# Performance work log

Hardware: AMD Instinct MI355X
Metric: run time of the kernel (lower is better)

The kernel has to match this reference:

```python
import jax, jax.numpy as jnp
import numpy as np

N_ATOMS = 300000
D_IN = 256


def setup_inputs() -> dict:
    key = jax.random.key(0)
    ks = jax.random.split(key, 8)

    def xavier(k, fan_in, fan_out):
        limit = float(np.sqrt(6.0 / (fan_in + fan_out)))
        return jax.random.uniform(k, (fan_in, fan_out), jnp.float32, -limit, limit)

    density = jax.random.normal(ks[0], (N_ATOMS, D_IN), jnp.float32)
    species = jax.random.randint(ks[1], (N_ATOMS,), -1, 10, jnp.int64)
    return {
        "density": density,
        "species": species,
        "W1": xavier(ks[2], 256, 512), "b1": jnp.zeros((512,), jnp.float32),
        "W2": xavier(ks[3], 512, 512), "b2": jnp.zeros((512,), jnp.float32),
        "W3": xavier(ks[4], 512, 256), "b3": jnp.zeros((256,), jnp.float32),
        "W4": xavier(ks[5], 256, 1),   "b4": jnp.zeros((1,), jnp.float32),
    }


def reference(density, species, W1, b1, W2, b2, W3, b3, W4, b4):
    # Equivalent to torch's nonzero-gather -> MLP -> scatter into zeros:
    # compute the MLP on all rows, then zero rows where species <= -0.5.
    h = jax.nn.silu(density @ W1 + b1)   # [N, 512]
    h = jax.nn.silu(h @ W2 + b2)         # [N, 512]
    h = jax.nn.silu(h @ W3 + b3)         # [N, 256]
    out = h @ W4 + b4                    # [N, 1]
    mask = species > -0.5                # valid atoms
    return jnp.where(mask[:, None], out, jnp.zeros((), out.dtype))
```

## Files before the change

kernel.cpp:

```cpp
#include <hip/hip_runtime.h>

typedef _Float16 half8 __attribute__((ext_vector_type(8)));
typedef _Float16 half4 __attribute__((ext_vector_type(4)));
typedef float f32x4 __attribute__((ext_vector_type(4)));
typedef float f32x16 __attribute__((ext_vector_type(16)));

#define NCHUNK_MAX 2048

__global__ void prep_compact(const float* __restrict__ W1, const float* __restrict__ W2,
                             const float* __restrict__ W3, const float* __restrict__ W4,
                             _Float16* __restrict__ wt1, _Float16* __restrict__ wt2,
                             _Float16* __restrict__ wt3, _Float16* __restrict__ w4h,
                             const int* __restrict__ species, int* __restrict__ idxloc,
                             int* __restrict__ cnt, float* __restrict__ out,
                             int natoms, int nprep) {
  __shared__ int wsum[4];
  if (blockIdx.x >= nprep) {
    const int c = blockIdx.x - nprep;
    const int i = c * 256 + threadIdx.x;
    const bool valid = (i < natoms) && (species[i] >= 0);
    const unsigned long long m = __ballot(valid);
    const int lane = threadIdx.x & 63, w = threadIdx.x >> 6;
    if (lane == 0) wsum[w] = (int)__popcll(m);
    __syncthreads();
    int base = 0;
#pragma unroll
    for (int k = 0; k < 4; ++k)
      if (k < w) base += wsum[k];
    if (valid) {
      int off = (int)__popcll(m & ((1ull << lane) - 1));
      idxloc[c * 256 + base + off] = i;
    } else if (i < natoms) {
      out[i] = 0.0f;
    }
    if (threadIdx.x == 0) cnt[c] = wsum[0] + wsum[1] + wsum[2] + wsum[3];
    return;
  }
  int idx = blockIdx.x * blockDim.x + threadIdx.x;
  if (idx < 512 * 256) {
    int k = idx >> 9, n = idx & 511;
    int off = (((n >> 5) * 16 + (k >> 4)) << 9) + (n & 31) * 8 + (((k >> 3) & 1) << 8) + (k & 7);
    wt1[off] = (_Float16)W1[idx];
    return;
  }
  int i2 = idx - 512 * 256;
  if (i2 < 512 * 512) {
    int k = i2 >> 9, n = i2 & 511;
    int off = (((n >> 5) * 32 + (k >> 4)) << 9) + (n & 31) * 8 + (((k >> 3) & 1) << 8) + (k & 7);
    wt2[off] = (_Float16)W2[i2];
    return;
  }
  int i3 = i2 - 512 * 512;
  if (i3 < 512 * 256) {
    int k = i3 >> 8, n = i3 & 255;
    int off = (((n >> 5) * 32 + (k >> 4)) << 9) + (n & 31) * 8 + (((k >> 3) & 1) << 8) + (k & 7);
    wt3[off] = (_Float16)W3[i3];
    return;
  }
  int i4 = i3 - 512 * 256;
  if (i4 < 256) w4h[i4] = (_Float16)W4[i4];
}

__device__ __forceinline__ float fast_silu(float s) {
  float e = __expf(-s);
  float d = 1.0f + e;
  float r;
  asm("v_rcp_f32 %0, %1" : "=v"(r) : "v"(d));
  return s * r;
}


#define MFMA(a, b, c) __builtin_amdgcn_mfma_f32_32x32x16_f16(a, b, c, 0, 0, 0)

template <int FT, int AT, int KS, int PIN, int POUT>
__device__ __forceinline__ void layer(const _Float16* __restrict__ wt,
                                      const float* __restrict__ bias,
                                      char* __restrict__ Hb,
                                      int wfeat, int lane) {
  const int lr = lane & 31;
  const int lh = lane >> 5;
  const int n0 = wfeat * (FT * 32);
  const int s0 = (lr & 31) << 4;
  const char* Bp = Hb + lr * PIN;
  const char* wp = (const char*)wt + (size_t)(wfeat * FT * KS) * 1024 + lh * 512 + lr * 16;

  f32x16 acc[FT][AT];
#pragma unroll
  for (int f = 0; f < FT; ++f)
#pragma unroll
    for (int rg = 0; rg < 4; ++rg) {
      const int feat = n0 + f * 32 + rg * 8 + lh * 4;
      const f32x4 bv = *(const f32x4*)(bias + feat);
#pragma unroll
      for (int a = 0; a < AT; ++a)
#pragma unroll
        for (int r = 0; r < 4; ++r) acc[f][a][rg * 4 + r] = bv[r];
    }

  half8 Af[FT], Ag[FT], Bf[AT], Bg[AT];
#pragma unroll
  for (int f = 0; f < FT; ++f) Af[f] = *(const half8*)(wp + f * (KS * 1024));
#pragma unroll
  for (int a = 0; a < AT; ++a)
    Bf[a] = *(const half8*)(Bp + a * 32 * PIN + ((lh * 16) ^ s0));

#pragma unroll 1
  for (int ks = 0; ks < KS - 2; ks += 2) {
#pragma unroll
    for (int f = 0; f < FT; ++f)
      Ag[f] = *(const half8*)(wp + f * (KS * 1024) + (ks + 1) * 1024);
#pragma unroll
    for (int a = 0; a < AT; ++a)
      Bg[a] = *(const half8*)(Bp + a * 32 * PIN + (((ks + 1) * 32 + lh * 16) ^ s0));
#pragma unroll
    for (int f = 0; f < FT; ++f)
#pragma unroll
      for (int a = 0; a < AT; ++a) acc[f][a] = MFMA(Af[f], Bf[a], acc[f][a]);
#pragma unroll
    for (int f = 0; f < FT; ++f)
      Af[f] = *(const half8*)(wp + f * (KS * 1024) + (ks + 2) * 1024);
#pragma unroll
    for (int a = 0; a < AT; ++a)
      Bf[a] = *(const half8*)(Bp + a * 32 * PIN + (((ks + 2) * 32 + lh * 16) ^ s0));
#pragma unroll
    for (int f = 0; f < FT; ++f)
#pragma unroll
      for (int a = 0; a < AT; ++a) acc[f][a] = MFMA(Ag[f], Bg[a], acc[f][a]);
  }
#pragma unroll
  for (int f = 0; f < FT; ++f)
    Ag[f] = *(const half8*)(wp + f * (KS * 1024) + (KS - 1) * 1024);
#pragma unroll
  for (int a = 0; a < AT; ++a)
    Bg[a] = *(const half8*)(Bp + a * 32 * PIN + ((((KS - 1) * 32) + lh * 16) ^ s0));
#pragma unroll
  for (int f = 0; f < FT; ++f)
#pragma unroll
    for (int a = 0; a < AT; ++a) acc[f][a] = MFMA(Af[f], Bf[a], acc[f][a]);
#pragma unroll
  for (int f = 0; f < FT; ++f)
#pragma unroll
    for (int a = 0; a < AT; ++a) acc[f][a] = MFMA(Ag[f], Bg[a], acc[f][a]);

#pragma unroll
  for (int f = 0; f < FT; ++f)
#pragma unroll
    for (int a = 0; a < AT; ++a)
#pragma unroll
      for (int j = 0; j < 16; ++j) acc[f][a][j] = fast_silu(acc[f][a][j]);

  __syncthreads();

#pragma unroll
  for (int f = 0; f < FT; ++f) {
#pragma unroll
    for (int rg = 0; rg < 4; ++rg) {
      const int feat = n0 + f * 32 + rg * 8 + lh * 4;
#pragma unroll
      for (int a = 0; a < AT; ++a) {
        half4 h;
#pragma unroll
        for (int r = 0; r < 4; ++r) h[r] = (_Float16)acc[f][a][rg * 4 + r];
        const int row = a * 32 + lr;
        *(half4*)(Hb + row * POUT + ((feat * 2) ^ ((row & 31) << 4))) = h;
      }
    }
  }
}

extern "C" __global__ void __launch_bounds__(512, 4)
mlp_kernel(const float* __restrict__ X, const int* __restrict__ species,
           const _Float16* __restrict__ wt1, const float* __restrict__ b1,
           const _Float16* __restrict__ wt2, const float* __restrict__ b2,
           const _Float16* __restrict__ wt3, const float* __restrict__ b3,
           const _Float16* __restrict__ w4h, const float* __restrict__ b4,
           float* __restrict__ out, int natoms,
           const int* __restrict__ idxloc, const int* __restrict__ cnt, int nchunks) {
  __shared__ __align__(16) char H[64 * 1024];
  __shared__ int prefixS[NCHUNK_MAX + 1];
  __shared__ int gidx[64];
  __shared__ int wtot[8];
  const int tid = threadIdx.x;
  const int lane = tid & 63;
  const int wid = tid >> 6;
  const long abase = (long)blockIdx.x * 64;

  int nvalid = natoms;
  if (idxloc) {
    int v[4];
    int tsum = 0;
#pragma unroll
    for (int j = 0; j < 4; ++j) {
      const int c = tid * 4 + j;
      v[j] = (c < nchunks) ? cnt[c] : 0;
      tsum += v[j];
    }
    int ws_ = tsum;
#pragma unroll
    for (int d = 1; d < 64; d <<= 1) {
      int o = __shfl_up(ws_, d);
      if (lane >= d) ws_ += o;
    }
    if (lane == 63) wtot[wid] = ws_;
    __syncthreads();
    int wbase = 0, tot = 0;
#pragma unroll
    for (int k = 0; k < 8; ++k) {
      if (k < wid) wbase += wtot[k];
      tot += wtot[k];
    }
    int run = wbase + ws_ - tsum;
#pragma unroll
    for (int j = 0; j < 4; ++j) {
      const int c = tid * 4 + j;
      if (c < nchunks) prefixS[c] = run;
      run += v[j];
    }
    if (tid == 0) prefixS[nchunks] = tot;
    nvalid = tot;
    __syncthreads();
    if (abase >= nvalid) return;
  }

  {
    const int r = tid >> 3, cg = tid & 7;
    long li = abase + r;
    const long lmax = (long)nvalid - 1;
    if (li > lmax) li = lmax;
    long g = li;
    if (idxloc) {
      int lo = 0, hi = nchunks - 1;
      while (lo < hi) {
        int mid = (lo + hi + 1) >> 1;
        if (prefixS[mid] <= (int)li) lo = mid; else hi = mid - 1;
      }
      g = idxloc[lo * 256 + ((int)li - prefixS[lo])];
      if (cg == 0) gidx[r] = (int)g;
    }
    const float* xp = X + g * 256;
    const int sw = (r & 31) << 4;
#pragma unroll
    for (int j = 0; j < 8; ++j) {
      const int colh = cg * 4 + j * 32;
      f32x4 v = *(const f32x4*)(xp + colh);
      half4 h;
#pragma unroll
      for (int e = 0; e < 4; ++e) h[e] = (_Float16)v[e];
      *(half4*)(H + r * 512 + ((colh * 2) ^ sw)) = h;
    }
  }
  __syncthreads();

  layer<2, 2, 16, 512, 1024>(wt1, b1, H, wid, lane);
  __syncthreads();
  layer<2, 2, 32, 1024, 1024>(wt2, b2, H, wid, lane);
  __syncthreads();
  layer<1, 2, 32, 1024, 1024>(wt3, b3, H, wid, lane);
  __syncthreads();

  const int atom = tid >> 3, part = tid & 7;
  const int sw = (atom & 31) << 4;
  const char* h3 = H + atom * 1024;
  const _Float16* w4p = w4h + part * 32;
  float sum = 0.0f;
#pragma unroll
  for (int j = 0; j < 4; ++j) {
    half8 h = *(const half8*)(h3 + ((part * 64 + j * 16) ^ sw));
    half8 w = *(const half8*)(w4p + j * 8);
#pragma unroll
    for (int e = 0; e < 8; ++e) sum += (float)h[e] * (float)w[e];
  }
  sum += __shfl_xor(sum, 1);
  sum += __shfl_xor(sum, 2);
  sum += __shfl_xor(sum, 4);
  if (part == 0) {
    const long li = abase + atom;
    if (li < nvalid) {
      float r = sum + b4[0];
      if (idxloc) {
        out[gidx[atom]] = r;
      } else {
        out[li] = (species[li] >= 0) ? r : 0.0f;
      }
    }
  }
}

extern "C" void kernel_launch(void* const* d_in, const int* in_sizes, int n_in,
                              void* d_out, int out_size, void* d_ws, size_t ws_size,
                              hipStream_t stream) {
  const float* X = (const float*)d_in[0];
  const int* species = (const int*)d_in[1];
  const float* W1 = (const float*)d_in[2];
  const float* b1 = (const float*)d_in[3];
  const float* W2 = (const float*)d_in[4];
  const float* b2 = (const float*)d_in[5];
  const float* W3 = (const float*)d_in[6];
  const float* b3 = (const float*)d_in[7];
  const float* W4 = (const float*)d_in[8];
  const float* b4 = (const float*)d_in[9];
  float* out = (float*)d_out;
  const int natoms = in_sizes[0] / 256;

  char* ws = (char*)d_ws;
  _Float16* wt1 = (_Float16*)(ws);
  _Float16* wt2 = (_Float16*)(ws + 262144);
  _Float16* wt3 = (_Float16*)(ws + 262144 + 524288);
  _Float16* w4h = (_Float16*)(ws + 262144 + 524288 + 262144);
  int* cnt = (int*)(ws + 1049088);
  int* idxloc = (int*)(ws + 1049088 + 8192);

  const int nchunks = (natoms + 255) / 256;
  const size_t ws_needed = 1049088 + 8192 + (size_t)natoms * 4;
  const bool use_compact = (ws_size >= ws_needed) && (nchunks <= NCHUNK_MAX);

  const int prep_total = 512 * 256 + 512 * 512 + 256 * 512 + 256;
  const int nprep = (prep_total + 255) / 256;
  const int nblk = nprep + (use_compact ? nchunks : 0);
  hipLaunchKernelGGL(prep_compact, dim3(nblk), dim3(256), 0, stream,
                     W1, W2, W3, W4, wt1, wt2, wt3, w4h,
                     species, idxloc, cnt, out, natoms, nprep);

  const int nblocks = (natoms + 63) / 64;
  hipLaunchKernelGGL(mlp_kernel, dim3(nblocks), dim3(512), 0, stream,
                     X, species, wt1, b1, wt2, b2, wt3, b3, w4h, b4, out, natoms,
                     use_compact ? idxloc : (const int*)nullptr,
                     use_compact ? (const int*)cnt : (const int*)nullptr, nchunks);
}
```

Before: 360.4 us.

## Fuse layer-3 GEMM with final dot product and enlarge compaction chunks

Layer 3 now uses a hand-written MFMA loop whose accumulators go straight through SiLU and are multiplied by W4 in registers. This replaces writing the layer-3 activations to LDS and reading them back for the output projection; per-warp partial sums are combined through a small LDS buffer instead. The compaction pass now uses 1024-atom chunks, so there are fewer chunk counts and the per-block prefix scan needs only one value per thread. The trade-off is more register pressure in the fused layer and a hand-scheduled software pipeline that has to stay correct.

```diff
diff --git a/kernel.cpp b/kernel.cpp
--- a/kernel.cpp
+++ b/kernel.cpp
@@ -5,7 +5,8 @@
 typedef float f32x4 __attribute__((ext_vector_type(4)));
 typedef float f32x16 __attribute__((ext_vector_type(16)));
 
-#define NCHUNK_MAX 2048
+#define CHUNK 1024
+#define NCHUNK_MAX 512
 
 __global__ void prep_compact(const float* __restrict__ W1, const float* __restrict__ W2,
                              const float* __restrict__ W3, const float* __restrict__ W4,
@@ -17,23 +18,29 @@
   __shared__ int wsum[4];
   if (blockIdx.x >= nprep) {
     const int c = blockIdx.x - nprep;
-    const int i = c * 256 + threadIdx.x;
-    const bool valid = (i < natoms) && (species[i] >= 0);
-    const unsigned long long m = __ballot(valid);
     const int lane = threadIdx.x & 63, w = threadIdx.x >> 6;
-    if (lane == 0) wsum[w] = (int)__popcll(m);
-    __syncthreads();
     int base = 0;
-#pragma unroll
-    for (int k = 0; k < 4; ++k)
-      if (k < w) base += wsum[k];
-    if (valid) {
-      int off = (int)__popcll(m & ((1ull << lane) - 1));
-      idxloc[c * 256 + base + off] = i;
-    } else if (i < natoms) {
-      out[i] = 0.0f;
-    }
-    if (threadIdx.x == 0) cnt[c] = wsum[0] + wsum[1] + wsum[2] + wsum[3];
+#pragma unroll 1
+    for (int j = 0; j < 4; ++j) {
+      const int i = c * CHUNK + j * 256 + threadIdx.x;
+      const bool valid = (i < natoms) && (species[i] >= 0);
+      const unsigned long long m = __ballot(valid);
+      if (lane == 0) wsum[w] = (int)__popcll(m);
+      __syncthreads();
+      int wb = base;
+#pragma unroll
+      for (int k = 0; k < 4; ++k)
+        if (k < w) wb += wsum[k];
+      if (valid) {
+        int off = (int)__popcll(m & ((1ull << lane) - 1));
+        idxloc[c * CHUNK + wb + off] = i;
+      } else if (i < natoms) {
+        out[i] = 0.0f;
+      }
+      base += wsum[0] + wsum[1] + wsum[2] + wsum[3];
+      __syncthreads();
+    }
+    if (threadIdx.x == 0) cnt[c] = base;
     return;
   }
   int idx = blockIdx.x * blockDim.x + threadIdx.x;
@@ -187,15 +194,8 @@
 
   int nvalid = natoms;
   if (idxloc) {
-    int v[4];
-    int tsum = 0;
-#pragma unroll
-    for (int j = 0; j < 4; ++j) {
-      const int c = tid * 4 + j;
-      v[j] = (c < nchunks) ? cnt[c] : 0;
-      tsum += v[j];
-    }
-    int ws_ = tsum;
+    int v = (tid < nchunks) ? cnt[tid] : 0;
+    int ws_ = v;
 #pragma unroll
     for (int d = 1; d < 64; d <<= 1) {
       int o = __shfl_up(ws_, d);
@@ -209,14 +209,7 @@
       if (k < wid) wbase += wtot[k];
       tot += wtot[k];
     }
-    int run = wbase + ws_ - tsum;
-#pragma unroll
-    for (int j = 0; j < 4; ++j) {
-      const int c = tid * 4 + j;
-      if (c < nchunks) prefixS[c] = run;
-      run += v[j];
-    }
-    if (tid == 0) prefixS[nchunks] = tot;
+    if (tid < nchunks) prefixS[tid] = wbase + ws_ - v;
     nvalid = tot;
     __syncthreads();
     if (abase >= nvalid) return;
@@ -234,7 +227,7 @@
         int mid = (lo + hi + 1) >> 1;
         if (prefixS[mid] <= (int)li) lo = mid; else hi = mid - 1;
       }
-      g = idxloc[lo * 256 + ((int)li - prefixS[lo])];
+      g = idxloc[lo * CHUNK + ((int)li - prefixS[lo])];
       if (cg == 0) gidx[r] = (int)g;
     }
     const float* xp = X + g * 256;
@@ -255,32 +248,96 @@
   __syncthreads();
   layer<2, 2, 32, 1024, 1024>(wt2, b2, H, wid, lane);
   __syncthreads();
-  layer<1, 2, 32, 1024, 1024>(wt3, b3, H, wid, lane);
-  __syncthreads();
-
-  const int atom = tid >> 3, part = tid & 7;
-  const int sw = (atom & 31) << 4;
-  const char* h3 = H + atom * 1024;
-  const _Float16* w4p = w4h + part * 32;
-  float sum = 0.0f;
-#pragma unroll
-  for (int j = 0; j < 4; ++j) {
-    half8 h = *(const half8*)(h3 + ((part * 64 + j * 16) ^ sw));
-    half8 w = *(const half8*)(w4p + j * 8);
-#pragma unroll
-    for (int e = 0; e < 8; ++e) sum += (float)h[e] * (float)w[e];
-  }
-  sum += __shfl_xor(sum, 1);
-  sum += __shfl_xor(sum, 2);
-  sum += __shfl_xor(sum, 4);
-  if (part == 0) {
-    const long li = abase + atom;
-    if (li < nvalid) {
-      float r = sum + b4[0];
-      if (idxloc) {
-        out[gidx[atom]] = r;
-      } else {
-        out[li] = (species[li] >= 0) ? r : 0.0f;
+
+  {
+    const int lr = lane & 31;
+    const int lh = lane >> 5;
+    const int n0 = wid * 32;
+    const int s0 = (lr & 31) << 4;
+    const char* Bp = H + lr * 1024;
+    const char* wp = (const char*)wt3 + (size_t)(wid * 32) * 1024 + lh * 512 + lr * 16;
+
+    f32x16 acc[2];
+#pragma unroll
+    for (int rg = 0; rg < 4; ++rg) {
+      const int feat = n0 + rg * 8 + lh * 4;
+      const f32x4 bv = *(const f32x4*)(b3 + feat);
+#pragma unroll
+      for (int a = 0; a < 2; ++a)
+#pragma unroll
+        for (int r = 0; r < 4; ++r) acc[a][rg * 4 + r] = bv[r];
+    }
+
+    half8 Af, Ag, Bf[2], Bg[2];
+    Af = *(const half8*)(wp);
+#pragma unroll
+    for (int a = 0; a < 2; ++a)
+      Bf[a] = *(const half8*)(Bp + a * 32 * 1024 + ((lh * 16) ^ s0));
+
+#pragma unroll 1
+    for (int ks = 0; ks < 30; ks += 2) {
+      Ag = *(const half8*)(wp + (ks + 1) * 1024);
+#pragma unroll
+      for (int a = 0; a < 2; ++a)
+        Bg[a] = *(const half8*)(Bp + a * 32 * 1024 + (((ks + 1) * 32 + lh * 16) ^ s0));
+#pragma unroll
+      for (int a = 0; a < 2; ++a) acc[a] = MFMA(Af, Bf[a], acc[a]);
+      Af = *(const half8*)(wp + (ks + 2) * 1024);
+#pragma unroll
+      for (int a = 0; a < 2; ++a)
+        Bf[a] = *(const half8*)(Bp + a * 32 * 1024 + (((ks + 2) * 32 + lh * 16) ^ s0));
+#pragma unroll
+      for (int a = 0; a < 2; ++a) acc[a] = MFMA(Ag, Bg[a], acc[a]);
+    }
+    Ag = *(const half8*)(wp + 31 * 1024);
+#pragma unroll
+    for (int a = 0; a < 2; ++a)
+      Bg[a] = *(const half8*)(Bp + a * 32 * 1024 + ((31 * 32 + lh * 16) ^ s0));
+#pragma unroll
+    for (int a = 0; a < 2; ++a) acc[a] = MFMA(Af, Bf[a], acc[a]);
+#pragma unroll
+    for (int a = 0; a < 2; ++a) acc[a] = MFMA(Ag, Bg[a], acc[a]);
+
+    float s[2] = {0.0f, 0.0f};
+#pragma unroll
+    for (int rg = 0; rg < 4; ++rg) {
+      half4 wv = *(const half4*)(w4h + n0 + rg * 8 + lh * 4);
+#pragma unroll
+      for (int r = 0; r < 4; ++r) {
+        const float wf = (float)wv[r];
+#pragma unroll
+        for (int a = 0; a < 2; ++a)
+          s[a] += fast_silu(acc[a][rg * 4 + r]) * wf;
+      }
+    }
+    s[0] += __shfl_xor(s[0], 32);
+    s[1] += __shfl_xor(s[1], 32);
+
+    __syncthreads();
+    float* P = (float*)H;
+    if (lh == 0) {
+      P[(0 * 32 + lr) * 8 + wid] = s[0];
+      P[(1 * 32 + lr) * 8 + wid] = s[1];
+    }
+  }
+  __syncthreads();
+
+  {
+    const float* P = (const float*)H;
+    const int atom = tid >> 3, part = tid & 7;
+    float sum = P[atom * 8 + part];
+    sum += __shfl_xor(sum, 1);
+    sum += __shfl_xor(sum, 2);
+    sum += __shfl_xor(sum, 4);
+    if (part == 0) {
+      const long li = abase + atom;
+      if (li < nvalid) {
+        float r = sum + b4[0];
+        if (idxloc) {
+          out[gidx[atom]] = r;
+        } else {
+          out[li] = (species[li] >= 0) ? r : 0.0f;
+        }
       }
     }
   }
@@ -308,10 +365,10 @@
   _Float16* wt3 = (_Float16*)(ws + 262144 + 524288);
   _Float16* w4h = (_Float16*)(ws + 262144 + 524288 + 262144);
   int* cnt = (int*)(ws + 1049088);
-  int* idxloc = (int*)(ws + 1049088 + 8192);
-
-  const int nchunks = (natoms + 255) / 256;
-  const size_t ws_needed = 1049088 + 8192 + (size_t)natoms * 4;
+  int* idxloc = (int*)(ws + 1049088 + 4096);
+
+  const int nchunks = (natoms + CHUNK - 1) / CHUNK;
+  const size_t ws_needed = 1049088 + 4096 + (size_t)nchunks * CHUNK * 4;
   const bool use_compact = (ws_size >= ws_needed) && (nchunks <= NCHUNK_MAX);
 
   const int prep_total = 512 * 256 + 512 * 512 + 256 * 512 + 256;
```

Measured after the change: 352.6 us. 1.02x faster.
